# Kernel optimization log

Measured on AMD Instinct MI355X. Metric: run time of the kernel, lower is better.

The kernel has to match this reference:

```python
import jax, jax.numpy as jnp
from jax import lax
import numpy as np

H = 50  # hidden size


def _lstm_layer(x, w_ih, w_hh, b_ih, b_hh):
    # x: [B, T, D_in]; returns full hidden sequence [B, T, H]
    B, T, _ = x.shape
    # precompute input contributions for all timesteps: [B, T, 4H]
    gx = jnp.einsum('bti,gi->btg', x, w_ih) + b_ih + b_hh
    gx_t = jnp.swapaxes(gx, 0, 1)  # [T, B, 4H]
    h0 = jnp.zeros((B, H), dtype=x.dtype)
    c0 = jnp.zeros((B, H), dtype=x.dtype)

    def step(carry, g_t):
        h, c = carry
        g = g_t + h @ w_hh.T  # [B, 4H]
        i, f, gg, o = jnp.split(g, 4, axis=-1)  # PyTorch gate order i,f,g,o
        i = jax.nn.sigmoid(i)
        f = jax.nn.sigmoid(f)
        gg = jnp.tanh(gg)
        o = jax.nn.sigmoid(o)
        c = f * c + i * gg
        h = o * jnp.tanh(c)
        return (h, c), h

    (_, _), hs = lax.scan(step, (h0, c0), gx_t)
    return jnp.swapaxes(hs, 0, 1)  # [B, T, H]


def setup_inputs() -> dict:
    key = jax.random.key(0)
    ks = jax.random.split(key, 12)
    s = 0.1  # weight init scale (~1/sqrt(H))
    return {
        'x': jax.random.normal(ks[0], (4096, 512, 1), dtype=jnp.float32),
        'w_ih0': jax.random.normal(ks[1], (4 * H, 1), dtype=jnp.float32) * s,
        'w_hh0': jax.random.normal(ks[2], (4 * H, H), dtype=jnp.float32) * s,
        'b_ih0': jax.random.normal(ks[3], (4 * H,), dtype=jnp.float32) * s,
        'b_hh0': jax.random.normal(ks[4], (4 * H,), dtype=jnp.float32) * s,
        'w_ih1': jax.random.normal(ks[5], (4 * H, H), dtype=jnp.float32) * s,
        'w_hh1': jax.random.normal(ks[6], (4 * H, H), dtype=jnp.float32) * s,
        'b_ih1': jax.random.normal(ks[7], (4 * H,), dtype=jnp.float32) * s,
        'b_hh1': jax.random.normal(ks[8], (4 * H,), dtype=jnp.float32) * s,
        'fc_w': jax.random.normal(ks[9], (1, H), dtype=jnp.float32) * s,
        'fc_b': jax.random.normal(ks[10], (1,), dtype=jnp.float32) * s,
    }


def reference(x, w_ih0, w_hh0, b_ih0, b_hh0, w_ih1, w_hh1, b_ih1, b_hh1, fc_w, fc_b):
    # 2-layer LSTM (dropout is identity in eval mode), last timestep -> Linear
    h1 = _lstm_layer(x, w_ih0, w_hh0, b_ih0, b_hh0)   # [B, T, H]
    h2 = _lstm_layer(h1, w_ih1, w_hh1, b_ih1, b_hh1)  # [B, T, H]
    last = h2[:, -1, :]                               # [B, H]
    return last @ fc_w.T + fc_b                       # [B, 1]
```

## Files before the change

kernel.cpp:

```cpp
#include <hip/hip_runtime.h>


#define HID 50
#define SEQ 512
#define NB 16
#define NTHREADS 832
#define XP 516

typedef _Float16 f16x8 __attribute__((ext_vector_type(8)));
typedef float    f32x4 __attribute__((ext_vector_type(4)));

#define LOG2E 1.44269504f

__device__ __forceinline__ float sigf(float x) {
    return __builtin_amdgcn_rcpf(1.0f + __builtin_amdgcn_exp2f(x * -LOG2E));
}
__device__ __forceinline__ float tanh_fast(float x) {
    return 1.0f - 2.0f * __builtin_amdgcn_rcpf(
        1.0f + __builtin_amdgcn_exp2f(x * (2.0f * LOG2E)));
}
__device__ __forceinline__ float lstm_cell(const f32x4 g, float& c) {
    const float ii = sigf(g[0]);
    const float ff = sigf(g[1]);
    const float gg = tanh_fast(g[2]);
    const float oo = sigf(g[3]);
    c = ff * c + ii * gg;
    return oo * tanh_fast(c);
}


__global__ __launch_bounds__(NTHREADS, 1)
void lstm2_fc_v9(const float* __restrict__ x,
                 const float* __restrict__ w_ih0,
                 const float* __restrict__ w_hh0,
                 const float* __restrict__ b_ih0,
                 const float* __restrict__ b_hh0,
                 const float* __restrict__ w_ih1,
                 const float* __restrict__ w_hh1,
                 const float* __restrict__ b_ih1,
                 const float* __restrict__ b_hh1,
                 const float* __restrict__ fc_w,
                 const float* __restrict__ fc_b,
                 float* __restrict__ out)
{
    __shared__ float xs[NB * XP];
    __shared__ f16x8 h1f[2][128];
    __shared__ f16x8 h2f[2][128];

    const int tid = threadIdx.x;
    const int b0  = blockIdx.x * NB;
    const int w   = tid >> 6;
    const int l15 = tid & 15;
    const int qq  = (tid >> 4) & 3;

    for (int idx = tid; idx < NB * 128; idx += NTHREADS) {
        const int b  = idx >> 7;
        const int t4 = idx & 127;
        *(float4*)&xs[b * XP + t4 * 4] =
            *(const float4*)&x[(size_t)(b0 + b) * SEQ + t4 * 4];
    }
    if (tid < NB) {
        const float4 z = {0.f, 0.f, 0.f, 0.f};
        *(float4*)&xs[tid * XP + 512] = z;
    }
    if (tid < 256) {
        f16x8 z = {};
        h1f[tid >> 7][tid & 127] = z;
        h2f[tid >> 7][tid & 127] = z;
    }

    const float* mats[3] = { w_hh0, w_ih1, w_hh1 };
    f16x8 wa[3][2];
    {
        const int  pA  = w * 16 + l15;
        const bool pok = (pA < 4 * HID);
        const int  n   = pok ? ((pA & 3) * HID + (pA >> 2)) : 0;
#pragma unroll
        for (int mi = 0; mi < 3; ++mi) {
#pragma unroll
            for (int kt = 0; kt < 2; ++kt) {
                f16x8 f;
#pragma unroll
                for (int j = 0; j < 8; ++j) {
                    const int k = kt * 32 + qq * 8 + j;
                    float v = 0.0f;
                    if (pok) {
                        if (k < HID)                     v = mats[mi][n * HID + k];
                        else if (mi == 0 && k == HID)    v = w_ih0[n];
                        else if (mi == 0 && k == HID+1)  v = b_ih0[n] + b_hh0[n];
                        else if (mi == 1 && k == HID+1)  v = b_ih1[n] + b_hh1[n];
                    }
                    f[j] = (_Float16)v;
                }
                wa[mi][kt] = f;
            }
        }
    }

    const int ju   = w * 4 + qq;
    const int wOff = ((((ju >> 5) * 4) + ((ju >> 3) & 3)) * 16 + l15) * 8 + (ju & 7);
    const int rdo  = qq * 16 + l15;
    const float* xrow = xs + l15 * XP;

    float c1 = 0.f, c2 = 0.f;

    __syncthreads();

    if (tid < NB) {
        _Float16* e0 = (_Float16*)&h1f[0][96 + tid];
        e0[2] = (_Float16)xs[tid * XP];
        e0[3] = (_Float16)1.0f;
        ((_Float16*)&h1f[1][96 + tid])[3] = (_Float16)1.0f;
    }
    __syncthreads();

    auto phase = [&](const f16x8* __restrict__ h1o, const f16x8* __restrict__ h2o,
                     f16x8* __restrict__ h1n, f16x8* __restrict__ h2n,
                     int p, bool doL1, bool doL2) {
        const f16x8 hb0 = h1o[rdo];
        const f16x8 hb1 = h1o[64 + rdo];
        _Float16 hw1, hw2;
        if (doL1) {
            f32x4 acc = {0.f, 0.f, 0.f, 0.f};
            acc = __builtin_amdgcn_mfma_f32_16x16x32_f16(wa[0][0], hb0, acc, 0, 0, 0);
            acc = __builtin_amdgcn_mfma_f32_16x16x32_f16(wa[0][1], hb1, acc, 0, 0, 0);
            hw1 = (_Float16)lstm_cell(acc, c1);
        }
        if (doL2) {
            const f16x8 sb0 = h2o[rdo];
            const f16x8 sb1 = h2o[64 + rdo];
            f32x4 acc = {0.f, 0.f, 0.f, 0.f};
            acc = __builtin_amdgcn_mfma_f32_16x16x32_f16(wa[1][0], hb0, acc, 0, 0, 0);
            acc = __builtin_amdgcn_mfma_f32_16x16x32_f16(wa[1][1], hb1, acc, 0, 0, 0);
            acc = __builtin_amdgcn_mfma_f32_16x16x32_f16(wa[2][0], sb0, acc, 0, 0, 0);
            acc = __builtin_amdgcn_mfma_f32_16x16x32_f16(wa[2][1], sb1, acc, 0, 0, 0);
            hw2 = (_Float16)lstm_cell(acc, c2);
        }
        if (doL1) {
            if (w < 12) {
                ((_Float16*)h1n)[wOff] = hw1;
            } else {
                if (qq < 2)       ((_Float16*)h1n)[wOff] = hw1;
                else if (qq == 2) ((_Float16*)h1n)[wOff] =
                                      (_Float16)xrow[p + 1];
            }
        }
        if (doL2) ((_Float16*)h2n)[wOff] = hw2;
        __syncthreads();
    };

    phase(h1f[0], h2f[0], h1f[1], h2f[1], 0, true, false);
#pragma unroll 1
    for (int p = 1; p <= 509; p += 2) {
        phase(h1f[1], h2f[1], h1f[0], h2f[0], p,     true, true);
        phase(h1f[0], h2f[0], h1f[1], h2f[1], p + 1, true, true);
    }
    phase(h1f[1], h2f[1], h1f[0], h2f[0], 511, true,  true);
    phase(h1f[0], h2f[0], h1f[1], h2f[1], 512, false, true);

    if (tid < NB) {
        const int m = tid;
        const _Float16* h2e = (const _Float16*)h2f[1];
        float s = fc_b[0];
        for (int j = 0; j < HID; ++j) {
            const int chunk = (((j >> 5) * 4) + ((j >> 3) & 3)) * 16 + m;
            s += fc_w[j] * (float)h2e[chunk * 8 + (j & 7)];
        }
        out[b0 + m] = s;
    }
}

extern "C" void kernel_launch(void* const* d_in, const int* in_sizes, int n_in,
                              void* d_out, int out_size, void* d_ws, size_t ws_size,
                              hipStream_t stream) {
    const float* x     = (const float*)d_in[0];
    const float* w_ih0 = (const float*)d_in[1];
    const float* w_hh0 = (const float*)d_in[2];
    const float* b_ih0 = (const float*)d_in[3];
    const float* b_hh0 = (const float*)d_in[4];
    const float* w_ih1 = (const float*)d_in[5];
    const float* w_hh1 = (const float*)d_in[6];
    const float* b_ih1 = (const float*)d_in[7];
    const float* b_hh1 = (const float*)d_in[8];
    const float* fc_w  = (const float*)d_in[9];
    const float* fc_b  = (const float*)d_in[10];
    float* out = (float*)d_out;

    const int B = in_sizes[0] / SEQ;

    lstm2_fc_v9<<<B / NB, NTHREADS, 0, stream>>>(
        x, w_ih0, w_hh0, b_ih0, b_hh0, w_ih1, w_hh1, b_ih1, b_hh1, fc_w, fc_b, out);
}
```

Before: 451.6 us.

## Halve waves per block by giving each wave two gate tiles

```diff
diff --git a/kernel.cpp b/kernel.cpp
--- a/kernel.cpp
+++ b/kernel.cpp
@@ -4,7 +4,7 @@
 #define HID 50
 #define SEQ 512
 #define NB 16
-#define NTHREADS 832
+#define NTHREADS 448
 #define XP 516
 
 typedef _Float16 f16x8 __attribute__((ext_vector_type(8)));
@@ -30,18 +30,18 @@
 
 
 __global__ __launch_bounds__(NTHREADS, 1)
-void lstm2_fc_v9(const float* __restrict__ x,
-                 const float* __restrict__ w_ih0,
-                 const float* __restrict__ w_hh0,
-                 const float* __restrict__ b_ih0,
-                 const float* __restrict__ b_hh0,
-                 const float* __restrict__ w_ih1,
-                 const float* __restrict__ w_hh1,
-                 const float* __restrict__ b_ih1,
-                 const float* __restrict__ b_hh1,
-                 const float* __restrict__ fc_w,
-                 const float* __restrict__ fc_b,
-                 float* __restrict__ out)
+void lstm2_fc_v10(const float* __restrict__ x,
+                  const float* __restrict__ w_ih0,
+                  const float* __restrict__ w_hh0,
+                  const float* __restrict__ b_ih0,
+                  const float* __restrict__ b_hh0,
+                  const float* __restrict__ w_ih1,
+                  const float* __restrict__ w_hh1,
+                  const float* __restrict__ b_ih1,
+                  const float* __restrict__ b_hh1,
+                  const float* __restrict__ fc_w,
+                  const float* __restrict__ fc_b,
+                  float* __restrict__ out)
 {
     __shared__ float xs[NB * XP];
     __shared__ f16x8 h1f[2][128];
@@ -52,6 +52,7 @@
     const int w   = tid >> 6;
     const int l15 = tid & 15;
     const int qq  = (tid >> 4) & 3;
+    const bool fat = (w < 6);
 
     for (int idx = tid; idx < NB * 128; idx += NTHREADS) {
         const int b  = idx >> 7;
@@ -70,9 +71,11 @@
     }
 
     const float* mats[3] = { w_hh0, w_ih1, w_hh1 };
-    f16x8 wa[3][2];
-    {
-        const int  pA  = w * 16 + l15;
+    f16x8 wa[3][2][2];
+#pragma unroll
+    for (int tt = 0; tt < 2; ++tt) {
+        const int  T   = 2 * w + tt;
+        const int  pA  = T * 16 + l15;
         const bool pok = (pA < 4 * HID);
         const int  n   = pok ? ((pA & 3) * HID + (pA >> 2)) : 0;
 #pragma unroll
@@ -92,17 +95,23 @@
                     }
                     f[j] = (_Float16)v;
                 }
-                wa[mi][kt] = f;
-            }
-        }
-    }
-
-    const int ju   = w * 4 + qq;
-    const int wOff = ((((ju >> 5) * 4) + ((ju >> 3) & 3)) * 16 + l15) * 8 + (ju & 7);
-    const int rdo  = qq * 16 + l15;
+                wa[mi][tt][kt] = f;
+            }
+        }
+    }
+
+    int wOff[2];
+#pragma unroll
+    for (int tt = 0; tt < 2; ++tt) {
+        const int ju = (2 * w + tt) * 4 + qq;
+        const int jc = ju & 63;
+        wOff[tt] = ((((jc >> 5) * 4) + ((jc >> 3) & 3)) * 16 + l15) * 8 + (jc & 7);
+    }
+    const int rdo = qq * 16 + l15;
     const float* xrow = xs + l15 * XP;
 
-    float c1 = 0.f, c2 = 0.f;
+    float c1[2] = {0.f, 0.f};
+    float c2[2] = {0.f, 0.f};
 
     __syncthreads();
 
@@ -119,33 +128,51 @@
                      int p, bool doL1, bool doL2) {
         const f16x8 hb0 = h1o[rdo];
         const f16x8 hb1 = h1o[64 + rdo];
-        _Float16 hw1, hw2;
+        _Float16 hw1[2], hw2[2];
         if (doL1) {
-            f32x4 acc = {0.f, 0.f, 0.f, 0.f};
-            acc = __builtin_amdgcn_mfma_f32_16x16x32_f16(wa[0][0], hb0, acc, 0, 0, 0);
-            acc = __builtin_amdgcn_mfma_f32_16x16x32_f16(wa[0][1], hb1, acc, 0, 0, 0);
-            hw1 = (_Float16)lstm_cell(acc, c1);
+#pragma unroll
+            for (int tt = 0; tt < 2; ++tt) {
+                if (tt == 0 || fat) {
+                    f32x4 acc = {0.f, 0.f, 0.f, 0.f};
+                    acc = __builtin_amdgcn_mfma_f32_16x16x32_f16(wa[0][tt][0], hb0, acc, 0, 0, 0);
+                    acc = __builtin_amdgcn_mfma_f32_16x16x32_f16(wa[0][tt][1], hb1, acc, 0, 0, 0);
+                    hw1[tt] = (_Float16)lstm_cell(acc, c1[tt]);
+                }
+            }
         }
         if (doL2) {
             const f16x8 sb0 = h2o[rdo];
             const f16x8 sb1 = h2o[64 + rdo];
-            f32x4 acc = {0.f, 0.f, 0.f, 0.f};
-            acc = __builtin_amdgcn_mfma_f32_16x16x32_f16(wa[1][0], hb0, acc, 0, 0, 0);
-            acc = __builtin_amdgcn_mfma_f32_16x16x32_f16(wa[1][1], hb1, acc, 0, 0, 0);
-            acc = __builtin_amdgcn_mfma_f32_16x16x32_f16(wa[2][0], sb0, acc, 0, 0, 0);
-            acc = __builtin_amdgcn_mfma_f32_16x16x32_f16(wa[2][1], sb1, acc, 0, 0, 0);
-            hw2 = (_Float16)lstm_cell(acc, c2);
+#pragma unroll
+            for (int tt = 0; tt < 2; ++tt) {
+                if (tt == 0 || fat) {
+                    f32x4 acc = {0.f, 0.f, 0.f, 0.f};
+                    acc = __builtin_amdgcn_mfma_f32_16x16x32_f16(wa[1][tt][0], hb0, acc, 0, 0, 0);
+                    acc = __builtin_amdgcn_mfma_f32_16x16x32_f16(wa[1][tt][1], hb1, acc, 0, 0, 0);
+                    acc = __builtin_amdgcn_mfma_f32_16x16x32_f16(wa[2][tt][0], sb0, acc, 0, 0, 0);
+                    acc = __builtin_amdgcn_mfma_f32_16x16x32_f16(wa[2][tt][1], sb1, acc, 0, 0, 0);
+                    hw2[tt] = (_Float16)lstm_cell(acc, c2[tt]);
+                }
+            }
         }
         if (doL1) {
-            if (w < 12) {
-                ((_Float16*)h1n)[wOff] = hw1;
+            if (fat) {
+                ((_Float16*)h1n)[wOff[0]] = hw1[0];
+                ((_Float16*)h1n)[wOff[1]] = hw1[1];
             } else {
-                if (qq < 2)       ((_Float16*)h1n)[wOff] = hw1;
-                else if (qq == 2) ((_Float16*)h1n)[wOff] =
+                if (qq < 2)       ((_Float16*)h1n)[wOff[0]] = hw1[0];
+                else if (qq == 2) ((_Float16*)h1n)[wOff[0]] =
                                       (_Float16)xrow[p + 1];
             }
         }
-        if (doL2) ((_Float16*)h2n)[wOff] = hw2;
+        if (doL2) {
+            if (fat) {
+                ((_Float16*)h2n)[wOff[0]] = hw2[0];
+                ((_Float16*)h2n)[wOff[1]] = hw2[1];
+            } else if (qq < 2) {
+                ((_Float16*)h2n)[wOff[0]] = hw2[0];
+            }
+        }
         __syncthreads();
     };
 
@@ -188,6 +215,6 @@
 
     const int B = in_sizes[0] / SEQ;
 
-    lstm2_fc_v9<<<B / NB, NTHREADS, 0, stream>>>(
+    lstm2_fc_v10<<<B / NB, NTHREADS, 0, stream>>>(
         x, w_ih0, w_hh0, b_ih0, b_hh0, w_ih1, w_hh1, b_ih1, b_hh1, fc_w, fc_b, out);
 }
```

Measured after the change: 548.2 us. 21.4% more time.

## Split layer-2 gate work across extra waves and prioritize dual-role waves

Applied to the files above, without the earlier changes.

```diff
diff --git a/kernel.cpp b/kernel.cpp
--- a/kernel.cpp
+++ b/kernel.cpp
@@ -4,7 +4,7 @@
 #define HID 50
 #define SEQ 512
 #define NB 16
-#define NTHREADS 832
+#define NTHREADS 1024
 #define XP 516
 
 typedef _Float16 f16x8 __attribute__((ext_vector_type(8)));
@@ -29,19 +29,19 @@
 }
 
 
-__global__ __launch_bounds__(NTHREADS, 1)
-void lstm2_fc_v9(const float* __restrict__ x,
-                 const float* __restrict__ w_ih0,
-                 const float* __restrict__ w_hh0,
-                 const float* __restrict__ b_ih0,
-                 const float* __restrict__ b_hh0,
-                 const float* __restrict__ w_ih1,
-                 const float* __restrict__ w_hh1,
-                 const float* __restrict__ b_ih1,
-                 const float* __restrict__ b_hh1,
-                 const float* __restrict__ fc_w,
-                 const float* __restrict__ fc_b,
-                 float* __restrict__ out)
+__global__ __launch_bounds__(NTHREADS)
+void lstm2_fc_v12(const float* __restrict__ x,
+                  const float* __restrict__ w_ih0,
+                  const float* __restrict__ w_hh0,
+                  const float* __restrict__ b_ih0,
+                  const float* __restrict__ b_hh0,
+                  const float* __restrict__ w_ih1,
+                  const float* __restrict__ w_hh1,
+                  const float* __restrict__ b_ih1,
+                  const float* __restrict__ b_hh1,
+                  const float* __restrict__ fc_w,
+                  const float* __restrict__ fc_b,
+                  float* __restrict__ out)
 {
     __shared__ float xs[NB * XP];
     __shared__ f16x8 h1f[2][128];
@@ -53,6 +53,14 @@
     const int l15 = tid & 15;
     const int qq  = (tid >> 4) & 3;
 
+    const bool dual  = (w <= 9);
+    const bool hasL1 = (w <= 12);
+    const bool hasL2 = dual || (w >= 13);
+    const int  tL1   = w;
+    const int  tL2   = dual ? w : (w - 3);
+
+    if (dual) __builtin_amdgcn_s_setprio(1);
+
     for (int idx = tid; idx < NB * 128; idx += NTHREADS) {
         const int b  = idx >> 7;
         const int t4 = idx & 127;
@@ -69,38 +77,48 @@
         h2f[tid >> 7][tid & 127] = z;
     }
 
-    const float* mats[3] = { w_hh0, w_ih1, w_hh1 };
-    f16x8 wa[3][2];
+    f16x8 wH0[2], wI1[2], wH1[2];
     {
-        const int  pA  = w * 16 + l15;
-        const bool pok = (pA < 4 * HID);
-        const int  n   = pok ? ((pA & 3) * HID + (pA >> 2)) : 0;
+        const int  p1  = tL1 * 16 + l15;
+        const bool ok1 = hasL1 && (p1 < 4 * HID);
+        const int  n1  = ok1 ? ((p1 & 3) * HID + (p1 >> 2)) : 0;
+        const int  p2  = tL2 * 16 + l15;
+        const bool ok2 = hasL2 && (p2 < 4 * HID);
+        const int  n2  = ok2 ? ((p2 & 3) * HID + (p2 >> 2)) : 0;
 #pragma unroll
-        for (int mi = 0; mi < 3; ++mi) {
+        for (int kt = 0; kt < 2; ++kt) {
+            f16x8 f0, f1, f2;
 #pragma unroll
-            for (int kt = 0; kt < 2; ++kt) {
-                f16x8 f;
-#pragma unroll
-                for (int j = 0; j < 8; ++j) {
-                    const int k = kt * 32 + qq * 8 + j;
-                    float v = 0.0f;
-                    if (pok) {
-                        if (k < HID)                     v = mats[mi][n * HID + k];
-                        else if (mi == 0 && k == HID)    v = w_ih0[n];
-                        else if (mi == 0 && k == HID+1)  v = b_ih0[n] + b_hh0[n];
-                        else if (mi == 1 && k == HID+1)  v = b_ih1[n] + b_hh1[n];
-                    }
-                    f[j] = (_Float16)v;
+            for (int j = 0; j < 8; ++j) {
+                const int k = kt * 32 + qq * 8 + j;
+                float v0 = 0.0f, v1 = 0.0f, v2 = 0.0f;
+                if (ok1) {
+                    if (k < HID)          v0 = w_hh0[n1 * HID + k];
+                    else if (k == HID)    v0 = w_ih0[n1];
+                    else if (k == HID+1)  v0 = b_ih0[n1] + b_hh0[n1];
                 }
-                wa[mi][kt] = f;
+                if (ok2) {
+                    if (k < HID)        { v1 = w_ih1[n2 * HID + k];
+                                          v2 = w_hh1[n2 * HID + k]; }
+                    else if (k == HID+1)  v1 = b_ih1[n2] + b_hh1[n2];
+                }
+                f0[j] = (_Float16)v0;
+                f1[j] = (_Float16)v1;
+                f2[j] = (_Float16)v2;
             }
-        }
-    }
-
-    const int ju   = w * 4 + qq;
-    const int wOff = ((((ju >> 5) * 4) + ((ju >> 3) & 3)) * 16 + l15) * 8 + (ju & 7);
-    const int rdo  = qq * 16 + l15;
+            wH0[kt] = f0;
+            wI1[kt] = f1;
+            wH1[kt] = f2;
+        }
+    }
+
+    const int juL1   = tL1 * 4 + qq;
+    const int juL2   = tL2 * 4 + qq;
+    const int wOffL1 = ((((juL1 >> 5) * 4) + ((juL1 >> 3) & 3)) * 16 + l15) * 8 + (juL1 & 7);
+    const int wOffL2 = ((((juL2 >> 5) * 4) + ((juL2 >> 3) & 3)) * 16 + l15) * 8 + (juL2 & 7);
+    const int rdo = qq * 16 + l15;
     const float* xrow = xs + l15 * XP;
+    const f32x4 z4 = {0.f, 0.f, 0.f, 0.f};
 
     float c1 = 0.f, c2 = 0.f;
 
@@ -119,33 +137,29 @@
                      int p, bool doL1, bool doL2) {
         const f16x8 hb0 = h1o[rdo];
         const f16x8 hb1 = h1o[64 + rdo];
-        _Float16 hw1, hw2;
-        if (doL1) {
-            f32x4 acc = {0.f, 0.f, 0.f, 0.f};
-            acc = __builtin_amdgcn_mfma_f32_16x16x32_f16(wa[0][0], hb0, acc, 0, 0, 0);
-            acc = __builtin_amdgcn_mfma_f32_16x16x32_f16(wa[0][1], hb1, acc, 0, 0, 0);
-            hw1 = (_Float16)lstm_cell(acc, c1);
-        }
-        if (doL2) {
+        if (hasL2 && doL2) {
             const f16x8 sb0 = h2o[rdo];
             const f16x8 sb1 = h2o[64 + rdo];
-            f32x4 acc = {0.f, 0.f, 0.f, 0.f};
-            acc = __builtin_amdgcn_mfma_f32_16x16x32_f16(wa[1][0], hb0, acc, 0, 0, 0);
-            acc = __builtin_amdgcn_mfma_f32_16x16x32_f16(wa[1][1], hb1, acc, 0, 0, 0);
-            acc = __builtin_amdgcn_mfma_f32_16x16x32_f16(wa[2][0], sb0, acc, 0, 0, 0);
-            acc = __builtin_amdgcn_mfma_f32_16x16x32_f16(wa[2][1], sb1, acc, 0, 0, 0);
-            hw2 = (_Float16)lstm_cell(acc, c2);
-        }
-        if (doL1) {
+            f32x4 acc;
+            acc = __builtin_amdgcn_mfma_f32_16x16x32_f16(wI1[0], hb0, z4,  0, 0, 0);
+            acc = __builtin_amdgcn_mfma_f32_16x16x32_f16(wI1[1], hb1, acc, 0, 0, 0);
+            acc = __builtin_amdgcn_mfma_f32_16x16x32_f16(wH1[0], sb0, acc, 0, 0, 0);
+            acc = __builtin_amdgcn_mfma_f32_16x16x32_f16(wH1[1], sb1, acc, 0, 0, 0);
+            ((_Float16*)h2n)[wOffL2] = (_Float16)lstm_cell(acc, c2);
+        }
+        if (hasL1 && doL1) {
+            f32x4 acc;
+            acc = __builtin_amdgcn_mfma_f32_16x16x32_f16(wH0[0], hb0, z4,  0, 0, 0);
+            acc = __builtin_amdgcn_mfma_f32_16x16x32_f16(wH0[1], hb1, acc, 0, 0, 0);
+            const _Float16 hw = (_Float16)lstm_cell(acc, c1);
             if (w < 12) {
-                ((_Float16*)h1n)[wOff] = hw1;
+                ((_Float16*)h1n)[wOffL1] = hw;
             } else {
-                if (qq < 2)       ((_Float16*)h1n)[wOff] = hw1;
-                else if (qq == 2) ((_Float16*)h1n)[wOff] =
+                if (qq < 2)       ((_Float16*)h1n)[wOffL1] = hw;
+                else if (qq == 2) ((_Float16*)h1n)[wOffL1] =
                                       (_Float16)xrow[p + 1];
             }
         }
-        if (doL2) ((_Float16*)h2n)[wOff] = hw2;
         __syncthreads();
     };
 
@@ -188,6 +202,6 @@
 
     const int B = in_sizes[0] / SEQ;
 
-    lstm2_fc_v9<<<B / NB, NTHREADS, 0, stream>>>(
+    lstm2_fc_v12<<<B / NB, NTHREADS, 0, stream>>>(
         x, w_ih0, w_hh0, b_ih0, b_hh0, w_ih1, w_hh1, b_ih1, b_hh1, fc_w, fc_b, out);
 }
```

After: 400.4 us. -11.3%, faster.
